# Optimization experiments

Hardware: AMD Instinct MI355X
Metric: run time of the kernel (lower is better)

## Reference

```python
import jax, jax.numpy as jnp
import numpy as np

N = 20000      # nodes
E = 320000     # edges (avg degree 16)
C = 64         # channels per degree
H = 8          # attention heads
DIM1 = 3       # degree-1 representation dim (2*1+1)
NUM_FEATURES = C * 1 + C * 3  # key_fiber.num_features = 256


def setup_inputs() -> dict:
    key = jax.random.key(0)
    ks = jax.random.split(key, 7)
    return {
        "value_0": jax.random.normal(ks[0], (E, C, 1), dtype=jnp.float32),
        "value_1": jax.random.normal(ks[1], (E, C, DIM1), dtype=jnp.float32),
        "key_0": jax.random.normal(ks[2], (E, C, 1), dtype=jnp.float32),
        "key_1": jax.random.normal(ks[3], (E, C, DIM1), dtype=jnp.float32),
        "query_0": jax.random.normal(ks[4], (N, C, 1), dtype=jnp.float32),
        "query_1": jax.random.normal(ks[5], (N, C, DIM1), dtype=jnp.float32),
        "dst": jax.random.randint(ks[6], (E,), 0, N),
    }


def _to_heads(f0, f1):
    # Fiber.to_attention_heads: per degree [n, C, dim] -> [n, H, (C//H)*dim], concat on last dim
    n = f0.shape[0]
    return jnp.concatenate([f0.reshape(n, H, -1), f1.reshape(n, H, -1)], axis=-1)


def reference(value_0, value_1, key_0, key_1, query_0, query_1, dst):
    k = _to_heads(key_0, key_1)        # [E, H, Dk]
    q = _to_heads(query_0, query_1)    # [N, H, Dk]
    # dgl.ops.e_dot_v: dot edge key with destination-node query, then scale
    logits = jnp.einsum('ehd,ehd->eh', k, q[dst]) / np.float32(np.sqrt(NUM_FEATURES))
    edge_prelogits = logits            # returned pre-softmax (scaled) as in original
    # edge_softmax over incoming edges of each destination node, per head
    m = jax.ops.segment_max(logits, dst, num_segments=N)           # [N, H]
    w = jnp.exp(logits - m[dst])                                   # [E, H]
    denom = jax.ops.segment_sum(w, dst, num_segments=N)            # [N, H]
    alpha = w / denom[dst]                                         # [E, H]

    def agg(v, dim):
        # value view: [E, H, C//H, dim]; weighted copy_e_sum -> [N, C, dim]
        vh = v.reshape(E, H, C // H, dim)
        out = jax.ops.segment_sum(alpha[:, :, None, None] * vh, dst, num_segments=N)
        return out.reshape(N, C, dim)

    out_0 = agg(value_0, 1)
    out_1 = agg(value_1, DIM1)
    return out_0, out_1, edge_prelogits
```

## Files before the change

### kernel.cpp

```cpp
#include <hip/hip_runtime.h>

#define N_NODES 20000
#define N_EDGES 320000
#define SLOTS  48


#define DOT4(a,b) ((a).x*(b).x + (a).y*(b).y + (a).z*(b).z + (a).w*(b).w)
#define FMA4(a,s,p) { (a).x += (s)*(p).x; (a).y += (s)*(p).y; (a).z += (s)*(p).z; (a).w += (s)*(p).w; }
#define RED4(a,m) { (a).x += __shfl_xor((a).x,m); (a).y += __shfl_xor((a).y,m); \
                    (a).z += __shfl_xor((a).z,m); (a).w += __shfl_xor((a).w,m); }

__global__ __launch_bounds__(256) void k_zero(int* __restrict__ p, int n)
{
    int i = blockIdx.x * 256 + threadIdx.x;
    if (i < n) p[i] = 0;
}

__global__ __launch_bounds__(256) void k_fill(
    const int* __restrict__ dst, int* __restrict__ counts, int* __restrict__ bucket)
{
    int e = blockIdx.x * 256 + threadIdx.x;
    if (e >= N_EDGES) return;
    int d = dst[e];
    int cnt = atomicAdd(&counts[d], 1);
    if (cnt < SLOTS) bucket[d * SLOTS + cnt] = e;
}

#define EPW 40
__global__ __launch_bounds__(256) void k_logits(
    const float* __restrict__ k0, const float* __restrict__ k1,
    const float* __restrict__ q0, const float* __restrict__ q1,
    const int* __restrict__ dst, float* __restrict__ logits,
    float* __restrict__ denom)
{
    int wave = blockIdx.x * 4 + (threadIdx.x >> 6);
    int l = threadIdx.x & 63;
    int j = l >> 3, h = l & 7;
    int e0 = wave * EPW;
    int e1 = min(e0 + EPW, N_EDGES);

    int off0 = h * 8 + 4 * j;
    int off1 = h * 24 + 4 * (j - 2);
    bool lo = (j < 2);

#pragma unroll 2
    for (int e = e0; e < e1; ++e) {
        int d = dst[e];
        const float4 kv = lo ? *(const float4*)(k0 + (size_t)e * 64  + off0)
                             : *(const float4*)(k1 + (size_t)e * 192 + off1);
        const float4 qv = lo ? *(const float4*)(q0 + (size_t)d * 64  + off0)
                             : *(const float4*)(q1 + (size_t)d * 192 + off1);
        float p = DOT4(kv, qv);
        p += __shfl_xor(p, 8);
        p += __shfl_xor(p, 16);
        p += __shfl_xor(p, 32);
        float x = p * 0.0625f;
        if (j == 0) {
            logits[(size_t)e * 8 + h] = x;
            atomicAdd(&denom[d * 8 + h], __expf(x));
        }
    }
}

#define B_BODY(BASE)                                                            \
{                                                                               \
    int sA = (BASE) + s2, sB = (BASE) + s2 + 4;                                 \
    int eA = bucket[bb + min(sA, deg - 1)];                                     \
    int eB = bucket[bb + min(sB, deg - 1)];                                     \
    const float* lrA = logits + (size_t)eA * 8;                                 \
    const float* lrB = logits + (size_t)eB * 8;                                 \
    float xA0 = lrA[hv0], xAa = lrA[hv1a], xAb = lrA[hv1b], xAc = lrA[hv1c];    \
    float xB0 = lrB[hv0], xBa = lrB[hv1a], xBb = lrB[hv1b], xBc = lrB[hv1c];    \
    const float4* r0A = (const float4*)(v0 + (size_t)eA * 64);                  \
    const float4* r1A = (const float4*)(v1 + (size_t)eA * 192);                 \
    const float4* r0B = (const float4*)(v0 + (size_t)eB * 64);                  \
    const float4* r1B = (const float4*)(v1 + (size_t)eB * 192);                 \
    float4 P0A = r0A[c], PaA = r1A[c], PbA = r1A[c + 16], PcA = r1A[c + 32];    \
    float4 P0B = r0B[c], PaB = r1B[c], PbB = r1B[c + 16], PcB = r1B[c + 32];    \
    float wA0 = __expf(xA0) * R0, wAa = __expf(xAa) * Ra;                       \
    float wAb = __expf(xAb) * Rb, wAc = __expf(xAc) * Rc;                       \
    float wB0 = __expf(xB0) * R0, wBa = __expf(xBa) * Ra;                       \
    float wBb = __expf(xBb) * Rb, wBc = __expf(xBc) * Rc;                       \
    if (sA >= deg) { wA0 = wAa = wAb = wAc = 0.f; }                             \
    if (sB >= deg) { wB0 = wBa = wBb = wBc = 0.f; }                             \
    FMA4(a0, wA0, P0A); FMA4(a1a, wAa, PaA); FMA4(a1b, wAb, PbA); FMA4(a1c, wAc, PcA); \
    FMA4(a0, wB0, P0B); FMA4(a1a, wBa, PaB); FMA4(a1b, wBb, PbB); FMA4(a1c, wBc, PcB); \
}

__global__ __launch_bounds__(256) void k_agg(
    const float* __restrict__ v0, const float* __restrict__ v1,
    const float* __restrict__ logits, const int* __restrict__ counts,
    const int* __restrict__ bucket, const float* __restrict__ denom,
    float* __restrict__ out0, float* __restrict__ out1)
{
    int w = threadIdx.x >> 6, l = threadIdx.x & 63;
    int node = blockIdx.x * 4 + w;
    int deg = counts[node];
    int bb = node * SLOTS;
    int s2 = l >> 4, c = l & 15;

    if (deg == 0) {
        if (l < 16) {
            float4 z = {0,0,0,0};
            ((float4*)(out0 + (size_t)node * 64))[c] = z;
            float4* o1 = (float4*)(out1 + (size_t)node * 192);
            o1[c] = z; o1[c + 16] = z; o1[c + 32] = z;
        }
        return;
    }

    int hv0  = c >> 1;
    int hv1a = c / 6;
    int hv1b = (c + 16) / 6;
    int hv1c = (c + 32) / 6;
    float R0 = 1.f / denom[node * 8 + hv0];
    float Ra = 1.f / denom[node * 8 + hv1a];
    float Rb = 1.f / denom[node * 8 + hv1b];
    float Rc = 1.f / denom[node * 8 + hv1c];

    float4 a0 = {0,0,0,0}, a1a = {0,0,0,0}, a1b = {0,0,0,0}, a1c = {0,0,0,0};

    B_BODY(0)
    if (deg > 8)  B_BODY(8)
    if (deg > 16) B_BODY(16)
    if (deg > 24) B_BODY(24)
    if (deg > 32) B_BODY(32)
    if (deg > 40) B_BODY(40)

    RED4(a0, 16);  RED4(a0, 32);
    RED4(a1a, 16); RED4(a1a, 32);
    RED4(a1b, 16); RED4(a1b, 32);
    RED4(a1c, 16); RED4(a1c, 32);

    if (l < 16) {
        float4* o0 = (float4*)(out0 + (size_t)node * 64);
        float4* o1 = (float4*)(out1 + (size_t)node * 192);
        o0[c]      = a0;
        o1[c]      = a1a;
        o1[c + 16] = a1b;
        o1[c + 32] = a1c;
    }
}

extern "C" void kernel_launch(void* const* d_in, const int* in_sizes, int n_in,
                              void* d_out, int out_size, void* d_ws, size_t ws_size,
                              hipStream_t stream) {
    const float* v0 = (const float*)d_in[0];
    const float* v1 = (const float*)d_in[1];
    const float* k0 = (const float*)d_in[2];
    const float* k1 = (const float*)d_in[3];
    const float* q0 = (const float*)d_in[4];
    const float* q1 = (const float*)d_in[5];
    const int*  dst = (const int*)d_in[6];

    float* out0   = (float*)d_out;
    float* out1   = out0 + (size_t)N_NODES * 64;
    float* logits = out1 + (size_t)N_NODES * 192;

    int*   wsI    = (int*)d_ws;
    int*   counts = wsI;
    float* denom  = (float*)(wsI + 20000);
    int*   bucket = wsI + 180000;

    k_zero   <<<704,  256, 0, stream>>>(wsI, 180000);
    k_fill   <<<1250, 256, 0, stream>>>(dst, counts, bucket);
    k_logits <<<2048, 256, 0, stream>>>(k0, k1, q0, q1, dst, logits, denom);
    k_agg    <<<5000, 256, 0, stream>>>(v0, v1, logits, counts, bucket, denom,
                                        out0, out1);
}
```

Before: 193.2 us.

## Fuse logits and aggregation into one node-centric kernel without atomics

The separate edge-parallel logits kernel, which used atomic denominator accumulation, and the node-parallel aggregation kernel are merged into one kernel. Each wave owns one destination node, loads its query once, walks the bucketed incoming edges, computes logits, exponentials and the per-head sum in registers, and writes the logits out as it goes. This removes the denominator buffer, its zeroing and atomics, and the logits re-read, and it shrinks the zero kernel. The trade-off is a serial per-edge loop with shuffle reductions in each wave, fewer edges handled in parallel per wave, and skipping of max-subtraction, as the code before also did.

Result: faster. 182.3 us (-5.7%).

```diff
diff --git a/kernel.cpp b/kernel.cpp
--- a/kernel.cpp
+++ b/kernel.cpp
@@ -7,8 +7,6 @@
 
 #define DOT4(a,b) ((a).x*(b).x + (a).y*(b).y + (a).z*(b).z + (a).w*(b).w)
 #define FMA4(a,s,p) { (a).x += (s)*(p).x; (a).y += (s)*(p).y; (a).z += (s)*(p).z; (a).w += (s)*(p).w; }
-#define RED4(a,m) { (a).x += __shfl_xor((a).x,m); (a).y += __shfl_xor((a).y,m); \
-                    (a).z += __shfl_xor((a).z,m); (a).w += __shfl_xor((a).w,m); }
 
 __global__ __launch_bounds__(256) void k_zero(int* __restrict__ p, int n)
 {
@@ -26,120 +24,75 @@
     if (cnt < SLOTS) bucket[d * SLOTS + cnt] = e;
 }
 
-#define EPW 40
-__global__ __launch_bounds__(256) void k_logits(
+__global__ __launch_bounds__(256) void k_fused(
+    const float* __restrict__ v0, const float* __restrict__ v1,
     const float* __restrict__ k0, const float* __restrict__ k1,
     const float* __restrict__ q0, const float* __restrict__ q1,
-    const int* __restrict__ dst, float* __restrict__ logits,
-    float* __restrict__ denom)
-{
-    int wave = blockIdx.x * 4 + (threadIdx.x >> 6);
-    int l = threadIdx.x & 63;
-    int j = l >> 3, h = l & 7;
-    int e0 = wave * EPW;
-    int e1 = min(e0 + EPW, N_EDGES);
-
-    int off0 = h * 8 + 4 * j;
-    int off1 = h * 24 + 4 * (j - 2);
-    bool lo = (j < 2);
-
-#pragma unroll 2
-    for (int e = e0; e < e1; ++e) {
-        int d = dst[e];
-        const float4 kv = lo ? *(const float4*)(k0 + (size_t)e * 64  + off0)
-                             : *(const float4*)(k1 + (size_t)e * 192 + off1);
-        const float4 qv = lo ? *(const float4*)(q0 + (size_t)d * 64  + off0)
-                             : *(const float4*)(q1 + (size_t)d * 192 + off1);
-        float p = DOT4(kv, qv);
-        p += __shfl_xor(p, 8);
-        p += __shfl_xor(p, 16);
-        p += __shfl_xor(p, 32);
-        float x = p * 0.0625f;
-        if (j == 0) {
-            logits[(size_t)e * 8 + h] = x;
-            atomicAdd(&denom[d * 8 + h], __expf(x));
-        }
-    }
-}
-
-#define B_BODY(BASE)                                                            \
-{                                                                               \
-    int sA = (BASE) + s2, sB = (BASE) + s2 + 4;                                 \
-    int eA = bucket[bb + min(sA, deg - 1)];                                     \
-    int eB = bucket[bb + min(sB, deg - 1)];                                     \
-    const float* lrA = logits + (size_t)eA * 8;                                 \
-    const float* lrB = logits + (size_t)eB * 8;                                 \
-    float xA0 = lrA[hv0], xAa = lrA[hv1a], xAb = lrA[hv1b], xAc = lrA[hv1c];    \
-    float xB0 = lrB[hv0], xBa = lrB[hv1a], xBb = lrB[hv1b], xBc = lrB[hv1c];    \
-    const float4* r0A = (const float4*)(v0 + (size_t)eA * 64);                  \
-    const float4* r1A = (const float4*)(v1 + (size_t)eA * 192);                 \
-    const float4* r0B = (const float4*)(v0 + (size_t)eB * 64);                  \
-    const float4* r1B = (const float4*)(v1 + (size_t)eB * 192);                 \
-    float4 P0A = r0A[c], PaA = r1A[c], PbA = r1A[c + 16], PcA = r1A[c + 32];    \
-    float4 P0B = r0B[c], PaB = r1B[c], PbB = r1B[c + 16], PcB = r1B[c + 32];    \
-    float wA0 = __expf(xA0) * R0, wAa = __expf(xAa) * Ra;                       \
-    float wAb = __expf(xAb) * Rb, wAc = __expf(xAc) * Rc;                       \
-    float wB0 = __expf(xB0) * R0, wBa = __expf(xBa) * Ra;                       \
-    float wBb = __expf(xBb) * Rb, wBc = __expf(xBc) * Rc;                       \
-    if (sA >= deg) { wA0 = wAa = wAb = wAc = 0.f; }                             \
-    if (sB >= deg) { wB0 = wBa = wBb = wBc = 0.f; }                             \
-    FMA4(a0, wA0, P0A); FMA4(a1a, wAa, PaA); FMA4(a1b, wAb, PbA); FMA4(a1c, wAc, PcA); \
-    FMA4(a0, wB0, P0B); FMA4(a1a, wBa, PaB); FMA4(a1b, wBb, PbB); FMA4(a1c, wBc, PcB); \
-}
-
-__global__ __launch_bounds__(256) void k_agg(
-    const float* __restrict__ v0, const float* __restrict__ v1,
-    const float* __restrict__ logits, const int* __restrict__ counts,
-    const int* __restrict__ bucket, const float* __restrict__ denom,
-    float* __restrict__ out0, float* __restrict__ out1)
+    const int* __restrict__ counts, const int* __restrict__ bucket,
+    float* __restrict__ logits, float* __restrict__ out0, float* __restrict__ out1)
 {
     int w = threadIdx.x >> 6, l = threadIdx.x & 63;
     int node = blockIdx.x * 4 + w;
-    int deg = counts[node];
-    int bb = node * SLOTS;
-    int s2 = l >> 4, c = l & 15;
+    int deg = min(counts[node], SLOTS);
+    const int* bk = bucket + node * SLOTS;
 
-    if (deg == 0) {
-        if (l < 16) {
-            float4 z = {0,0,0,0};
-            ((float4*)(out0 + (size_t)node * 64))[c] = z;
-            float4* o1 = (float4*)(out1 + (size_t)node * 192);
-            o1[c] = z; o1[c + 16] = z; o1[c + 32] = z;
+    int j = l >> 3, h = l & 7;
+    bool lo = (j < 2);
+    int koff = lo ? (h * 8 + 4 * j) : (h * 24 + 4 * (j - 2));
+    int hv = (l < 16) ? (l >> 1) : (l - 16) / 6;
+
+    float4 q4 = lo ? *(const float4*)(q0 + (size_t)node * 64  + koff)
+                   : *(const float4*)(q1 + (size_t)node * 192 + koff);
+
+    int eReg = (l < deg) ? bk[l] : 0;
+
+    float S = 0.f;
+    float4 acc = {0, 0, 0, 0};
+
+#pragma unroll 2
+    for (int i = 0; i < deg; i += 2) {
+        int iB = min(i + 1, deg - 1);
+        bool okB = (i + 1) < deg;
+        int eA = __shfl(eReg, i);
+        int eB = __shfl(eReg, iB);
+
+        float4 kA = lo ? *(const float4*)(k0 + (size_t)eA * 64  + koff)
+                       : *(const float4*)(k1 + (size_t)eA * 192 + koff);
+        float4 kB = lo ? *(const float4*)(k0 + (size_t)eB * 64  + koff)
+                       : *(const float4*)(k1 + (size_t)eB * 192 + koff);
+        float4 vA = (l < 16) ? ((const float4*)(v0 + (size_t)eA * 64))[l]
+                             : ((const float4*)(v1 + (size_t)eA * 192))[l - 16];
+        float4 vB = (l < 16) ? ((const float4*)(v0 + (size_t)eB * 64))[l]
+                             : ((const float4*)(v1 + (size_t)eB * 192))[l - 16];
+
+        float pA = DOT4(kA, q4);
+        float pB = DOT4(kB, q4);
+        pA += __shfl_xor(pA, 8);  pB += __shfl_xor(pB, 8);
+        pA += __shfl_xor(pA, 16); pB += __shfl_xor(pB, 16);
+        pA += __shfl_xor(pA, 32); pB += __shfl_xor(pB, 32);
+        float xA = pA * 0.0625f;
+        float xB = pB * 0.0625f;
+        float exA = __expf(xA);
+        float exB = okB ? __expf(xB) : 0.f;
+        S += exA + exB;
+
+        if (j == 0) {
+            logits[(size_t)eA * 8 + h] = xA;
+            if (okB) logits[(size_t)eB * 8 + h] = xB;
         }
-        return;
+
+        float aA = __shfl(exA, hv);
+        float aB = __shfl(exB, hv);
+        FMA4(acc, aA, vA);
+        FMA4(acc, aB, vB);
     }
 
-    int hv0  = c >> 1;
-    int hv1a = c / 6;
-    int hv1b = (c + 16) / 6;
-    int hv1c = (c + 32) / 6;
-    float R0 = 1.f / denom[node * 8 + hv0];
-    float Ra = 1.f / denom[node * 8 + hv1a];
-    float Rb = 1.f / denom[node * 8 + hv1b];
-    float Rc = 1.f / denom[node * 8 + hv1c];
+    float rinv = (S > 0.f) ? 1.f / S : 0.f;
+    float rv = __shfl(rinv, hv);
+    acc.x *= rv; acc.y *= rv; acc.z *= rv; acc.w *= rv;
 
-    float4 a0 = {0,0,0,0}, a1a = {0,0,0,0}, a1b = {0,0,0,0}, a1c = {0,0,0,0};
-
-    B_BODY(0)
-    if (deg > 8)  B_BODY(8)
-    if (deg > 16) B_BODY(16)
-    if (deg > 24) B_BODY(24)
-    if (deg > 32) B_BODY(32)
-    if (deg > 40) B_BODY(40)
-
-    RED4(a0, 16);  RED4(a0, 32);
-    RED4(a1a, 16); RED4(a1a, 32);
-    RED4(a1b, 16); RED4(a1b, 32);
-    RED4(a1c, 16); RED4(a1c, 32);
-
-    if (l < 16) {
-        float4* o0 = (float4*)(out0 + (size_t)node * 64);
-        float4* o1 = (float4*)(out1 + (size_t)node * 192);
-        o0[c]      = a0;
-        o1[c]      = a1a;
-        o1[c + 16] = a1b;
-        o1[c + 32] = a1c;
-    }
+    if (l < 16) ((float4*)(out0 + (size_t)node * 64))[l]       = acc;
+    else        ((float4*)(out1 + (size_t)node * 192))[l - 16] = acc;
 }
 
 extern "C" void kernel_launch(void* const* d_in, const int* in_sizes, int n_in,
@@ -157,14 +110,12 @@
     float* out1   = out0 + (size_t)N_NODES * 64;
     float* logits = out1 + (size_t)N_NODES * 192;
 
-    int*   wsI    = (int*)d_ws;
-    int*   counts = wsI;
-    float* denom  = (float*)(wsI + 20000);
-    int*   bucket = wsI + 180000;
+    int* wsI    = (int*)d_ws;
+    int* counts = wsI;
+    int* bucket = wsI + 20000;
 
-    k_zero   <<<704,  256, 0, stream>>>(wsI, 180000);
-    k_fill   <<<1250, 256, 0, stream>>>(dst, counts, bucket);
-    k_logits <<<2048, 256, 0, stream>>>(k0, k1, q0, q1, dst, logits, denom);
-    k_agg    <<<5000, 256, 0, stream>>>(v0, v1, logits, counts, bucket, denom,
-                                        out0, out1);
+    k_zero  <<<79,   256, 0, stream>>>(counts, N_NODES);
+    k_fill  <<<1250, 256, 0, stream>>>(dst, counts, bucket);
+    k_fused <<<5000, 256, 0, stream>>>(v0, v1, k0, k1, q0, q1,
+                                       counts, bucket, logits, out0, out1);
 }
```

## Compute logits per destination node via buckets, replacing atomic denominator accumulation

Applied to the files above, without the earlier changes.

The logits kernel now runs one wavefront per destination node and walks its bucketed edge list. The query row is loaded once into registers, and the per-head dot products are reduced through shared memory. The softmax denominator is summed in registers and stored as a reciprocal table, so the atomicAdd traffic and the large zeroing of the denominator buffer go away, and the aggregation kernel no longer does divides. In exchange, key rows are gathered by scattered edge index instead of being streamed, and block-wide syncs plus shared-memory staging are added.

Result: no change. 191.2 us (-1.0%).

```diff
diff --git a/kernel.cpp b/kernel.cpp
--- a/kernel.cpp
+++ b/kernel.cpp
@@ -26,40 +26,92 @@
     if (cnt < SLOTS) bucket[d * SLOTS + cnt] = e;
 }
 
-#define EPW 40
+
+#define LOADR(R, E, A0, A1, A2, A3)                                             \
+{                                                                               \
+    int g = base + s2 + 4 * (R);                                                \
+    int idx = min(g, dm1);                                                      \
+    E = bucket[bb + idx];                                                       \
+    const float4* kr0 = (const float4*)(k0 + (size_t)E * 64);                   \
+    const float4* kr1 = (const float4*)(k1 + (size_t)E * 192);                  \
+    A0 = kr0[c]; A1 = kr1[c]; A2 = kr1[c + 16]; A3 = kr1[c + 32];               \
+}
+
 __global__ __launch_bounds__(256) void k_logits(
     const float* __restrict__ k0, const float* __restrict__ k1,
     const float* __restrict__ q0, const float* __restrict__ q1,
-    const int* __restrict__ dst, float* __restrict__ logits,
-    float* __restrict__ denom)
-{
-    int wave = blockIdx.x * 4 + (threadIdx.x >> 6);
-    int l = threadIdx.x & 63;
-    int j = l >> 3, h = l & 7;
-    int e0 = wave * EPW;
-    int e1 = min(e0 + EPW, N_EDGES);
-
-    int off0 = h * 8 + 4 * j;
-    int off1 = h * 24 + 4 * (j - 2);
-    bool lo = (j < 2);
-
-#pragma unroll 2
-    for (int e = e0; e < e1; ++e) {
-        int d = dst[e];
-        const float4 kv = lo ? *(const float4*)(k0 + (size_t)e * 64  + off0)
-                             : *(const float4*)(k1 + (size_t)e * 192 + off1);
-        const float4 qv = lo ? *(const float4*)(q0 + (size_t)d * 64  + off0)
-                             : *(const float4*)(q1 + (size_t)d * 192 + off1);
-        float p = DOT4(kv, qv);
-        p += __shfl_xor(p, 8);
-        p += __shfl_xor(p, 16);
-        p += __shfl_xor(p, 32);
-        float x = p * 0.0625f;
-        if (j == 0) {
-            logits[(size_t)e * 8 + h] = x;
-            atomicAdd(&denom[d * 8 + h], __expf(x));
+    const int* __restrict__ counts, const int* __restrict__ bucket,
+    float* __restrict__ logits, float* __restrict__ Rtab)
+{
+    __shared__ float4 part4[4 * 256];
+    int w = threadIdx.x >> 6, l = threadIdx.x & 63;
+    int node = blockIdx.x * 4 + w;
+    int deg = min(counts[node], SLOTS);
+    int bb = node * SLOTS;
+    int dm1 = (deg > 0) ? deg - 1 : 0;
+
+    int s2 = l >> 4, c = l & 15;
+    int sl = l >> 3, h = l & 7;
+
+    const float4* q0f = (const float4*)(q0 + (size_t)node * 64);
+    const float4* q1f = (const float4*)(q1 + (size_t)node * 192);
+    float4 Q0 = q0f[c], Q1a = q1f[c], Q1b = q1f[c + 16], Q1c = q1f[c + 32];
+
+    float* pf = (float*)part4 + (size_t)w * 1024;
+    int ro[8];
+    ro[0] = (2 * h) * 4 + 0;
+    ro[1] = (2 * h + 1) * 4 + 0;
+#pragma unroll
+    for (int kk = 0; kk < 6; ++kk) {
+        int i = 6 * h + kk;
+        ro[2 + kk] = (i & 15) * 4 + 1 + (i >> 4);
+    }
+
+    float S = 0.f;
+
+#pragma unroll
+    for (int pass = 0; pass < 3; ++pass) {
+        int base = pass * 16;
+        bool act = base < deg;
+
+        if (act) {
+            int e0, e1, e2, e3;
+            float4 A00, A01, A02, A03, A10, A11, A12, A13;
+            float4 A20, A21, A22, A23, A30, A31, A32, A33;
+            LOADR(0, e0, A00, A01, A02, A03)
+            LOADR(1, e1, A10, A11, A12, A13)
+            LOADR(2, e2, A20, A21, A22, A23)
+            LOADR(3, e3, A30, A31, A32, A33)
+            float4* wp = part4 + w * 256;
+            wp[(s2     ) * 16 + c] = make_float4(DOT4(A00,Q0), DOT4(A01,Q1a), DOT4(A02,Q1b), DOT4(A03,Q1c));
+            wp[(s2 +  4) * 16 + c] = make_float4(DOT4(A10,Q0), DOT4(A11,Q1a), DOT4(A12,Q1b), DOT4(A13,Q1c));
+            wp[(s2 +  8) * 16 + c] = make_float4(DOT4(A20,Q0), DOT4(A21,Q1a), DOT4(A22,Q1b), DOT4(A23,Q1c));
+            wp[(s2 + 12) * 16 + c] = make_float4(DOT4(A30,Q0), DOT4(A31,Q1a), DOT4(A32,Q1b), DOT4(A33,Q1c));
         }
-    }
+        __syncthreads();
+        if (act) {
+#pragma unroll
+            for (int m = 0; m < 2; ++m) {
+                int srow = sl + 8 * m;
+                int slot = base + srow;
+                if (slot < deg) {
+                    const float* row = pf + srow * 64;
+                    float x = row[ro[0]] + row[ro[1]] + row[ro[2]] + row[ro[3]]
+                            + row[ro[4]] + row[ro[5]] + row[ro[6]] + row[ro[7]];
+                    x *= 0.0625f;
+                    int e = bucket[bb + slot];
+                    logits[(size_t)e * 8 + h] = x;
+                    S += __expf(x);
+                }
+            }
+        }
+        __syncthreads();
+    }
+
+    S += __shfl_xor(S, 8);
+    S += __shfl_xor(S, 16);
+    S += __shfl_xor(S, 32);
+    if (l < 8 && deg > 0) Rtab[node * 8 + l] = 1.f / S;
 }
 
 #define B_BODY(BASE)                                                            \
@@ -90,12 +142,12 @@
 __global__ __launch_bounds__(256) void k_agg(
     const float* __restrict__ v0, const float* __restrict__ v1,
     const float* __restrict__ logits, const int* __restrict__ counts,
-    const int* __restrict__ bucket, const float* __restrict__ denom,
+    const int* __restrict__ bucket, const float* __restrict__ Rtab,
     float* __restrict__ out0, float* __restrict__ out1)
 {
     int w = threadIdx.x >> 6, l = threadIdx.x & 63;
     int node = blockIdx.x * 4 + w;
-    int deg = counts[node];
+    int deg = min(counts[node], SLOTS);
     int bb = node * SLOTS;
     int s2 = l >> 4, c = l & 15;
 
@@ -113,10 +165,10 @@
     int hv1a = c / 6;
     int hv1b = (c + 16) / 6;
     int hv1c = (c + 32) / 6;
-    float R0 = 1.f / denom[node * 8 + hv0];
-    float Ra = 1.f / denom[node * 8 + hv1a];
-    float Rb = 1.f / denom[node * 8 + hv1b];
-    float Rc = 1.f / denom[node * 8 + hv1c];
+    float R0 = Rtab[node * 8 + hv0];
+    float Ra = Rtab[node * 8 + hv1a];
+    float Rb = Rtab[node * 8 + hv1b];
+    float Rc = Rtab[node * 8 + hv1c];
 
     float4 a0 = {0,0,0,0}, a1a = {0,0,0,0}, a1b = {0,0,0,0}, a1c = {0,0,0,0};
 
@@ -159,12 +211,13 @@
 
     int*   wsI    = (int*)d_ws;
     int*   counts = wsI;
-    float* denom  = (float*)(wsI + 20000);
-    int*   bucket = wsI + 180000;
-
-    k_zero   <<<704,  256, 0, stream>>>(wsI, 180000);
+    int*   bucket = wsI + 20000;
+    float* Rtab   = (float*)(wsI + 980000);
+
+    k_zero   <<<79,   256, 0, stream>>>(counts, N_NODES);
     k_fill   <<<1250, 256, 0, stream>>>(dst, counts, bucket);
-    k_logits <<<2048, 256, 0, stream>>>(k0, k1, q0, q1, dst, logits, denom);
-    k_agg    <<<5000, 256, 0, stream>>>(v0, v1, logits, counts, bucket, denom,
+    k_logits <<<5000, 256, 0, stream>>>(k0, k1, q0, q1, counts, bucket,
+                                        logits, Rtab);
+    k_agg    <<<5000, 256, 0, stream>>>(v0, v1, logits, counts, bucket, Rtab,
                                         out0, out1);
 }
```

## Compute logits per destination node from buckets, replacing atomic denominators with reciprocal table

Applied to the files above, without the earlier changes.

The logits kernel is now node-centric. One 384-thread block per destination node walks that node's bucketed edges, loads the query once, and reduces the exp-sum per head through shared memory. It writes a reciprocal-denominator table, which removes the atomicAdd traffic on the denominators and the larger zero-fill of that array. The cost is 20000 small blocks, many of them with idle waves, since six waves cover up to 48 slots while the average degree is 16. Key loads are now gathered by edge index instead of streamed in order.

Result: slower. 229.0 us (+18.6%).

```diff
diff --git a/kernel.cpp b/kernel.cpp
--- a/kernel.cpp
+++ b/kernel.cpp
@@ -26,39 +26,49 @@
     if (cnt < SLOTS) bucket[d * SLOTS + cnt] = e;
 }
 
-#define EPW 40
-__global__ __launch_bounds__(256) void k_logits(
+__global__ __launch_bounds__(384) void k_logits(
     const float* __restrict__ k0, const float* __restrict__ k1,
     const float* __restrict__ q0, const float* __restrict__ q1,
-    const int* __restrict__ dst, float* __restrict__ logits,
-    float* __restrict__ denom)
+    const int* __restrict__ counts, const int* __restrict__ bucket,
+    float* __restrict__ logits, float* __restrict__ Rtab)
 {
-    int wave = blockIdx.x * 4 + (threadIdx.x >> 6);
-    int l = threadIdx.x & 63;
-    int j = l >> 3, h = l & 7;
-    int e0 = wave * EPW;
-    int e1 = min(e0 + EPW, N_EDGES);
+    __shared__ float sp[6 * 8];
+    int node = blockIdx.x;
+    int wv = threadIdx.x >> 6, l = threadIdx.x & 63;
+    int deg = min(counts[node], SLOTS);
+    int base = wv * 8;
 
-    int off0 = h * 8 + 4 * j;
-    int off1 = h * 24 + 4 * (j - 2);
-    bool lo = (j < 2);
+    int f = l >> 3, h = l & 7;
+    bool lo = (f < 2);
+    int koff = lo ? (h * 8 + 4 * f) : (h * 24 + 4 * (f - 2));
 
-#pragma unroll 2
-    for (int e = e0; e < e1; ++e) {
-        int d = dst[e];
-        const float4 kv = lo ? *(const float4*)(k0 + (size_t)e * 64  + off0)
-                             : *(const float4*)(k1 + (size_t)e * 192 + off1);
-        const float4 qv = lo ? *(const float4*)(q0 + (size_t)d * 64  + off0)
-                             : *(const float4*)(q1 + (size_t)d * 192 + off1);
-        float p = DOT4(kv, qv);
-        p += __shfl_xor(p, 8);
-        p += __shfl_xor(p, 16);
-        p += __shfl_xor(p, 32);
-        float x = p * 0.0625f;
-        if (j == 0) {
-            logits[(size_t)e * 8 + h] = x;
-            atomicAdd(&denom[d * 8 + h], __expf(x));
+    float S = 0.f;
+    if (base < deg) {
+        float4 q4 = lo ? *(const float4*)(q0 + (size_t)node * 64  + koff)
+                       : *(const float4*)(q1 + (size_t)node * 192 + koff);
+        int eReg = bucket[node * SLOTS + min(base + (l & 7), deg - 1)];
+
+#pragma unroll
+        for (int i = 0; i < 8; ++i) {
+            int e = __shfl(eReg, i);
+            float4 k4 = lo ? *(const float4*)(k0 + (size_t)e * 64  + koff)
+                           : *(const float4*)(k1 + (size_t)e * 192 + koff);
+            float p = DOT4(k4, q4);
+            p += __shfl_xor(p, 8);
+            p += __shfl_xor(p, 16);
+            p += __shfl_xor(p, 32);
+            float x = p * 0.0625f;
+            bool ok = base + i < deg;
+            if (ok && l < 8) logits[(size_t)e * 8 + h] = x;
+            S += ok ? __expf(x) : 0.f;
         }
+    }
+    if (l < 8) sp[wv * 8 + h] = S;
+    __syncthreads();
+    if (threadIdx.x < 8) {
+        float d = sp[threadIdx.x] + sp[8 + threadIdx.x] + sp[16 + threadIdx.x]
+                + sp[24 + threadIdx.x] + sp[32 + threadIdx.x] + sp[40 + threadIdx.x];
+        Rtab[node * 8 + threadIdx.x] = (d > 0.f) ? 1.f / d : 0.f;
     }
 }
 
@@ -90,12 +100,12 @@
 __global__ __launch_bounds__(256) void k_agg(
     const float* __restrict__ v0, const float* __restrict__ v1,
     const float* __restrict__ logits, const int* __restrict__ counts,
-    const int* __restrict__ bucket, const float* __restrict__ denom,
+    const int* __restrict__ bucket, const float* __restrict__ Rtab,
     float* __restrict__ out0, float* __restrict__ out1)
 {
     int w = threadIdx.x >> 6, l = threadIdx.x & 63;
     int node = blockIdx.x * 4 + w;
-    int deg = counts[node];
+    int deg = min(counts[node], SLOTS);
     int bb = node * SLOTS;
     int s2 = l >> 4, c = l & 15;
 
@@ -113,10 +123,10 @@
     int hv1a = c / 6;
     int hv1b = (c + 16) / 6;
     int hv1c = (c + 32) / 6;
-    float R0 = 1.f / denom[node * 8 + hv0];
-    float Ra = 1.f / denom[node * 8 + hv1a];
-    float Rb = 1.f / denom[node * 8 + hv1b];
-    float Rc = 1.f / denom[node * 8 + hv1c];
+    float R0 = Rtab[node * 8 + hv0];
+    float Ra = Rtab[node * 8 + hv1a];
+    float Rb = Rtab[node * 8 + hv1b];
+    float Rc = Rtab[node * 8 + hv1c];
 
     float4 a0 = {0,0,0,0}, a1a = {0,0,0,0}, a1b = {0,0,0,0}, a1c = {0,0,0,0};
 
@@ -159,12 +169,13 @@
 
     int*   wsI    = (int*)d_ws;
     int*   counts = wsI;
-    float* denom  = (float*)(wsI + 20000);
-    int*   bucket = wsI + 180000;
+    int*   bucket = wsI + 20000;
+    float* Rtab   = (float*)(wsI + 980000);
 
-    k_zero   <<<704,  256, 0, stream>>>(wsI, 180000);
-    k_fill   <<<1250, 256, 0, stream>>>(dst, counts, bucket);
-    k_logits <<<2048, 256, 0, stream>>>(k0, k1, q0, q1, dst, logits, denom);
-    k_agg    <<<5000, 256, 0, stream>>>(v0, v1, logits, counts, bucket, denom,
-                                        out0, out1);
+    k_zero   <<<79,    256, 0, stream>>>(counts, N_NODES);
+    k_fill   <<<1250,  256, 0, stream>>>(dst, counts, bucket);
+    k_logits <<<20000, 384, 0, stream>>>(k0, k1, q0, q1, counts, bucket,
+                                         logits, Rtab);
+    k_agg    <<<5000,  256, 0, stream>>>(v0, v1, logits, counts, bucket, Rtab,
+                                         out0, out1);
 }
```
